# Kernel optimization log

Hardware: AMD Instinct MI355X
Metric: run time of the kernel (lower is better)

The kernel has to match this reference:

```python
import jax, jax.numpy as jnp
import numpy as np

N_HEAD = 12
NEG_INF = -10000.0


def setup_inputs() -> dict:
    key = jax.random.key(0)
    k1, k2, k3 = jax.random.split(key, 3)
    B, S, D = 8, 1024, 768
    std = 0.01
    return {
        "hidden_states": jax.random.normal(k1, (B, S, D), dtype=jnp.float32),
        "Wqkv": jax.random.normal(k2, (D, 3 * D), dtype=jnp.float32) * std,
        "bqkv": jnp.zeros((3 * D,), dtype=jnp.float32),
        "Wout": jax.random.normal(k3, (D, D), dtype=jnp.float32) * std,
        "bout": jnp.zeros((D,), dtype=jnp.float32),
    }


def reference(hidden_states, Wqkv, bqkv, Wout, bout):
    B, S, D = hidden_states.shape
    H = N_HEAD
    hd = D // H
    # fused QKV projection
    qkv = hidden_states @ Wqkv + bqkv  # [B,S,3D]
    qkv = qkv.reshape(B, S, 3, H, hd)
    q, k, v = qkv[:, :, 0], qkv[:, :, 1], qkv[:, :, 2]  # [B,S,H,hd]
    q = q.transpose(0, 2, 1, 3)  # [B,H,S,hd]
    k = k.transpose(0, 2, 1, 3)
    v = v.transpose(0, 2, 1, 3)
    scale = 1.0 / jnp.sqrt(jnp.asarray(hd, dtype=hidden_states.dtype))
    scores = jnp.einsum("bhqd,bhkd->bhqk", q, k) * scale  # [B,H,S,S]
    causal = jnp.tril(jnp.ones((S, S), dtype=bool))[None, None]
    scores = jnp.where(causal, scores, jnp.asarray(NEG_INF, scores.dtype))
    probs = jax.nn.softmax(scores, axis=-1)
    # dropout is identity in eval/deterministic mode
    attn = jnp.einsum("bhqk,bhkd->bhqd", probs, v)  # [B,H,S,hd]
    attn = attn.transpose(0, 2, 1, 3).reshape(B, S, D)
    return attn @ Wout + bout
```

## Files before the change

### kernel.cpp

```cpp
#include <hip/hip_runtime.h>
#include <hip/hip_bf16.h>

#define B_   8
#define S_   1024
#define D_   768
#define H_   12
#define HD_  64
#define BS_  (B_*S_)
#define N3_  (3*D_)

typedef __attribute__((ext_vector_type(8))) short short8;
typedef __attribute__((ext_vector_type(4))) float f32x4;

__device__ __forceinline__ short8 ld8(const __hip_bfloat16* p) {
    return *reinterpret_cast<const short8*>(p);
}
__device__ __forceinline__ void st8(__hip_bfloat16* p, short8 v) {
    *reinterpret_cast<short8*>(p) = v;
}
__device__ __forceinline__ f32x4 mfma16(short8 a, short8 b, f32x4 c) {
    return __builtin_amdgcn_mfma_f32_16x16x32_bf16(a, b, c, 0, 0, 0);
}
__device__ __forceinline__ void async16(const __hip_bfloat16* g, __hip_bfloat16* l) {
    __builtin_amdgcn_global_load_lds((const __attribute__((address_space(1))) void*)g,
                                     (__attribute__((address_space(3))) void*)l,
                                     16, 0, 0);
}
__device__ __forceinline__ float fast_exp2(float x) {
#if __has_builtin(__builtin_amdgcn_exp2f)
    return __builtin_amdgcn_exp2f(x);
#else
    return __expf(x * 0.69314718056f);
#endif
}

__global__ void cast_f32_bf16(const float* __restrict__ in,
                              __hip_bfloat16* __restrict__ out, int n) {
    int i = (blockIdx.x * blockDim.x + threadIdx.x) * 4;
    if (i + 3 < n) {
        float4 v = *reinterpret_cast<const float4*>(in + i);
        out[i + 0] = __float2bfloat16(v.x);
        out[i + 1] = __float2bfloat16(v.y);
        out[i + 2] = __float2bfloat16(v.z);
        out[i + 3] = __float2bfloat16(v.w);
    }
}

__global__ void transpose_cast(const float* __restrict__ in,
                               __hip_bfloat16* __restrict__ out, int R, int C) {
    __shared__ float tile[32][33];
    int c0 = blockIdx.x * 32, r0 = blockIdx.y * 32;
    for (int i = threadIdx.y; i < 32; i += 8) {
        tile[i][threadIdx.x] = in[(size_t)(r0 + i) * C + c0 + threadIdx.x];
    }
    __syncthreads();
    for (int i = threadIdx.y; i < 32; i += 8) {
        out[(size_t)(c0 + i) * R + r0 + threadIdx.x] =
            __float2bfloat16(tile[threadIdx.x][i]);
    }
}

__global__ __launch_bounds__(256)
void gemm_qkv(const __hip_bfloat16* __restrict__ A,
              const __hip_bfloat16* __restrict__ Bt,
              const float* __restrict__ bqkv,
              __hip_bfloat16* __restrict__ Qb,
              __hip_bfloat16* __restrict__ Kb,
              __hip_bfloat16* __restrict__ Vtb) {
    __shared__ __align__(16) char smem[49152];
    __hip_bfloat16* Ct = (__hip_bfloat16*)smem;

    int tid = threadIdx.x, wave = tid >> 6, lane = tid & 63;
    int ln = lane & 15, quad = lane >> 4;
    int mb = blockIdx.y * 128, nb = blockIdx.x * 128;
    int wm = (wave >> 1) * 64, wn = (wave & 1) * 64;

    f32x4 acc[4][4];
#pragma unroll
    for (int i = 0; i < 4; ++i)
#pragma unroll
        for (int j = 0; j < 4; ++j) acc[i][j] = (f32x4){0.f, 0.f, 0.f, 0.f};

    auto stage = [&](int k, int bufoff) {
        __hip_bfloat16* Asb = (__hip_bfloat16*)(smem + bufoff);
        __hip_bfloat16* Bsb = Asb + 128 * 32;
#pragma unroll
        for (int it = 0; it < 2; ++it) {
            int c = it * 256 + tid;
            int row = c >> 2, cc = c & 3;
            int csw = cc ^ ((row >> 1) & 3);
            async16(A + (size_t)(mb + row) * D_ + k + csw * 8,
                    Asb + it * 2048 + wave * 512);
            async16(Bt + (size_t)(nb + row) * D_ + k + csw * 8,
                    Bsb + it * 2048 + wave * 512);
        }
    };

    auto compute = [&](int bufoff) {
        __hip_bfloat16* As = (__hip_bfloat16*)(smem + bufoff);
        __hip_bfloat16* Bs = As + 128 * 32;
        short8 a[4], b[4];
#pragma unroll
        for (int i = 0; i < 4; ++i) {
            int row = wm + i * 16 + ln;
            a[i] = ld8(As + row * 32 + ((quad ^ ((row >> 1) & 3)) << 3));
        }
#pragma unroll
        for (int j = 0; j < 4; ++j) {
            int row = wn + j * 16 + ln;
            b[j] = ld8(Bs + row * 32 + ((quad ^ ((row >> 1) & 3)) << 3));
        }
#pragma unroll
        for (int i = 0; i < 4; ++i)
#pragma unroll
            for (int j = 0; j < 4; ++j)
                acc[i][j] = mfma16(a[i], b[j], acc[i][j]);
    };

    stage(0, 0);
    stage(32, 16384);
    int cb = 0;
    for (int k = 0; k < D_ - 32; k += 32) {
        asm volatile("s_waitcnt vmcnt(4)" ::: "memory");
        asm volatile("s_barrier" ::: "memory");
        if (k + 64 < D_) {
            int sb = cb + 32768; if (sb >= 49152) sb -= 49152;
            stage(k + 64, sb);
        }
        compute(cb);
        cb += 16384; if (cb >= 49152) cb = 0;
    }
    asm volatile("s_waitcnt vmcnt(0)" ::: "memory");
    asm volatile("s_barrier" ::: "memory");
    compute(cb);
    __syncthreads();

    int which = blockIdx.x / 6;
    int nbr = nb - which * D_;
    float qscale = (which == 0) ? (0.125f * 1.44269504089f) : 1.f;

#pragma unroll
    for (int j = 0; j < 4; ++j) {
        int col = wn + j * 16 + ln;
        float bias = bqkv[nb + col];
#pragma unroll
        for (int i = 0; i < 4; ++i)
#pragma unroll
            for (int r = 0; r < 4; ++r) {
                int row = wm + i * 16 + quad * 4 + r;
                __hip_bfloat16 v = __float2bfloat16((acc[i][j][r] + bias) * qscale);
                if (which != 2) Ct[row * 132 + col] = v;
                else            Ct[col * 132 + row] = v;
            }
    }
    __syncthreads();

    int bb = mb >> 10, sb = mb & 1023;
    if (which != 2) {
        __hip_bfloat16* dst = (which == 0) ? Qb : Kb;
#pragma unroll
        for (int it = 0; it < 8; ++it) {
            int cc = it * 256 + tid;
            int row = cc >> 4, c8 = cc & 15;
            short8 v = ld8(Ct + row * 132 + c8 * 8);
            int gcol = nbr + c8 * 8;
            int h = gcol >> 6, d = gcol & 63;
            int s = sb + row;
            st8(dst + (((size_t)(bb * H_ + h)) * S_ + s) * HD_ + d, v);
        }
    } else {
#pragma unroll
        for (int it = 0; it < 8; ++it) {
            int cc = it * 256 + tid;
            int drow = cc >> 4, s8 = cc & 15;
            short8 v = ld8(Ct + drow * 132 + s8 * 8);
            int gd = nbr + drow;
            int h = gd >> 6, d = gd & 63;
            st8(Vtb + ((size_t)(bb * H_ + h) * HD_ + d) * S_ + sb + s8 * 8, v);
        }
    }
}

__global__ __launch_bounds__(256, 3)
void attn_flash3(const __hip_bfloat16* __restrict__ Q,
                 const __hip_bfloat16* __restrict__ K,
                 const __hip_bfloat16* __restrict__ Vt,
                 __hip_bfloat16* __restrict__ attnbf) {
    __shared__ __hip_bfloat16 Kbuf[2][64 * 64];
    __shared__ __hip_bfloat16 Vbuf[2][64 * 64];
    __shared__ __hip_bfloat16 Pbuf[4][32 * 72];

    int bh = blockIdx.y;
    int ip = blockIdx.x;
    int tid = threadIdx.x;
    int wave = tid >> 6, lane = tid & 63;
    int ln = lane & 15, quad = lane >> 4;
    int strip = (wave < 2) ? ip : (15 - ip);
    int qrow0 = strip * 64 + (wave & 1) * 32;

    const __hip_bfloat16* Qbh = Q + (size_t)bh * S_ * HD_;
    const __hip_bfloat16* Kbh = K + (size_t)bh * S_ * HD_;
    const __hip_bfloat16* Vbh = Vt + (size_t)bh * HD_ * S_;

    short8 aq[2][2];
#pragma unroll
    for (int rt = 0; rt < 2; ++rt)
#pragma unroll
        for (int ks = 0; ks < 2; ++ks)
            aq[rt][ks] = ld8(Qbh + (size_t)(qrow0 + rt * 16 + ln) * HD_ +
                             ks * 32 + quad * 8);

    f32x4 o[2][4];
    float l_run[2][4];
#pragma unroll
    for (int rt = 0; rt < 2; ++rt)
#pragma unroll
        for (int n = 0; n < 4; ++n) {
            o[rt][n] = (f32x4){0.f, 0.f, 0.f, 0.f};
            l_run[rt][n] = 0.f;
        }

    int last_kt = 15 - ip;

    auto stage = [&](int kt, int buf) {
        const __hip_bfloat16* gK = Kbh + (size_t)kt * 64 * HD_;
#pragma unroll
        for (int it = 0; it < 2; ++it) {
            int p = it * 256 + tid;
            int row = p >> 3;
            int csw = (p & 7) ^ (row & 7);
            async16(gK + row * HD_ + csw * 8,
                    &Kbuf[buf][it * 2048 + wave * 512]);
            async16(Vbh + (size_t)row * S_ + kt * 64 + csw * 8,
                    &Vbuf[buf][it * 2048 + wave * 512]);
        }
    };

    stage(0, 0);
    __syncthreads();
    int cur = 0;

    for (int kt = 0; kt <= last_kt; ++kt) {
        int kbase = kt * 64;
        if (kt < last_kt) stage(kt + 1, cur ^ 1);

        if (kbase <= qrow0 + 31) {
            const __hip_bfloat16* Kc = Kbuf[cur];
            const __hip_bfloat16* Vc = Vbuf[cur];

            f32x4 s[2][4];
#pragma unroll
            for (int rt = 0; rt < 2; ++rt)
#pragma unroll
                for (int j = 0; j < 4; ++j) s[rt][j] = (f32x4){0.f, 0.f, 0.f, 0.f};
#pragma unroll
            for (int j = 0; j < 4; ++j) {
                int row = j * 16 + ln;
#pragma unroll
                for (int ks = 0; ks < 2; ++ks) {
                    short8 bk = ld8(&Kc[row * 64 +
                                        (((ks * 4 + quad) ^ (row & 7)) << 3)]);
#pragma unroll
                    for (int rt = 0; rt < 2; ++rt)
                        s[rt][j] = mfma16(aq[rt][ks], bk, s[rt][j]);
                }
            }

            if (kbase + 63 > qrow0) {
#pragma unroll
                for (int rt = 0; rt < 2; ++rt)
#pragma unroll
                    for (int j = 0; j < 4; ++j) {
                        int key = kbase + j * 16 + ln;
#pragma unroll
                        for (int r = 0; r < 4; ++r) {
                            int q = qrow0 + rt * 16 + quad * 4 + r;
                            if (key > q) s[rt][j][r] = -INFINITY;
                        }
                    }
            }

#pragma unroll
            for (int rt = 0; rt < 2; ++rt)
#pragma unroll
                for (int j = 0; j < 4; ++j)
#pragma unroll
                    for (int r = 0; r < 4; ++r)
                        s[rt][j][r] = fast_exp2(s[rt][j][r]);
#pragma unroll
            for (int rt = 0; rt < 2; ++rt)
#pragma unroll
                for (int r = 0; r < 4; ++r)
                    l_run[rt][r] += (s[rt][0][r] + s[rt][1][r]) +
                                    (s[rt][2][r] + s[rt][3][r]);

#pragma unroll
            for (int rt = 0; rt < 2; ++rt)
#pragma unroll
                for (int j = 0; j < 4; ++j)
#pragma unroll
                    for (int r = 0; r < 4; ++r)
                        Pbuf[wave][(rt * 16 + quad * 4 + r) * 72 + j * 16 + ln] =
                            __float2bfloat16(s[rt][j][r]);
            asm volatile("s_waitcnt lgkmcnt(0)" ::: "memory");

            short8 ap[2][2];
#pragma unroll
            for (int rt = 0; rt < 2; ++rt)
#pragma unroll
                for (int ks = 0; ks < 2; ++ks)
                    ap[rt][ks] = ld8(&Pbuf[wave][(rt * 16 + ln) * 72 +
                                                 ks * 32 + quad * 8]);

#pragma unroll
            for (int n = 0; n < 4; ++n) {
                int row = n * 16 + ln;
#pragma unroll
                for (int ks = 0; ks < 2; ++ks) {
                    short8 bv = ld8(&Vc[row * 64 +
                                        (((ks * 4 + quad) ^ (row & 7)) << 3)]);
#pragma unroll
                    for (int rt = 0; rt < 2; ++rt)
                        o[rt][n] = mfma16(ap[rt][ks], bv, o[rt][n]);
                }
            }
        }

        __syncthreads();
        cur ^= 1;
    }

    int bb = bh / H_, h = bh - bb * H_;
#pragma unroll
    for (int rt = 0; rt < 2; ++rt)
#pragma unroll
        for (int r = 0; r < 4; ++r) {
            float l = l_run[rt][r];
            l += __shfl_xor(l, 1);
            l += __shfl_xor(l, 2);
            l += __shfl_xor(l, 4);
            l += __shfl_xor(l, 8);
            float inv = 1.f / l;
            int row = qrow0 + rt * 16 + quad * 4 + r;
#pragma unroll
            for (int n = 0; n < 4; ++n) {
                int col = h * 64 + n * 16 + ln;
                attnbf[((size_t)bb * S_ + row) * D_ + col] =
                    __float2bfloat16(o[rt][n][r] * inv);
            }
        }
}

__global__ __launch_bounds__(256)
void gemm_out(const __hip_bfloat16* __restrict__ A,
              const __hip_bfloat16* __restrict__ Bt,
              const float* __restrict__ bias,
              float* __restrict__ Cout) {
    __shared__ __align__(16) char smem[49152];

    int tid = threadIdx.x, wave = tid >> 6, lane = tid & 63;
    int ln = lane & 15, quad = lane >> 4;
    int mb = blockIdx.y * 128, nb = blockIdx.x * 128;
    int wm = (wave >> 1) * 64, wn = (wave & 1) * 64;

    f32x4 acc[4][4];
#pragma unroll
    for (int i = 0; i < 4; ++i)
#pragma unroll
        for (int j = 0; j < 4; ++j) acc[i][j] = (f32x4){0.f, 0.f, 0.f, 0.f};

    auto stage = [&](int k, int bufoff) {
        __hip_bfloat16* Asb = (__hip_bfloat16*)(smem + bufoff);
        __hip_bfloat16* Bsb = Asb + 128 * 32;
#pragma unroll
        for (int it = 0; it < 2; ++it) {
            int c = it * 256 + tid;
            int row = c >> 2, cc = c & 3;
            int csw = cc ^ ((row >> 1) & 3);
            async16(A + (size_t)(mb + row) * D_ + k + csw * 8,
                    Asb + it * 2048 + wave * 512);
            async16(Bt + (size_t)(nb + row) * D_ + k + csw * 8,
                    Bsb + it * 2048 + wave * 512);
        }
    };

    auto compute = [&](int bufoff) {
        __hip_bfloat16* As = (__hip_bfloat16*)(smem + bufoff);
        __hip_bfloat16* Bs = As + 128 * 32;
        short8 a[4], b[4];
#pragma unroll
        for (int i = 0; i < 4; ++i) {
            int row = wm + i * 16 + ln;
            a[i] = ld8(As + row * 32 + ((quad ^ ((row >> 1) & 3)) << 3));
        }
#pragma unroll
        for (int j = 0; j < 4; ++j) {
            int row = wn + j * 16 + ln;
            b[j] = ld8(Bs + row * 32 + ((quad ^ ((row >> 1) & 3)) << 3));
        }
#pragma unroll
        for (int i = 0; i < 4; ++i)
#pragma unroll
            for (int j = 0; j < 4; ++j)
                acc[i][j] = mfma16(a[i], b[j], acc[i][j]);
    };

    stage(0, 0);
    stage(32, 16384);
    int cb = 0;
    for (int k = 0; k < D_ - 32; k += 32) {
        asm volatile("s_waitcnt vmcnt(4)" ::: "memory");
        asm volatile("s_barrier" ::: "memory");
        if (k + 64 < D_) {
            int sb = cb + 32768; if (sb >= 49152) sb -= 49152;
            stage(k + 64, sb);
        }
        compute(cb);
        cb += 16384; if (cb >= 49152) cb = 0;
    }
    asm volatile("s_waitcnt vmcnt(0)" ::: "memory");
    asm volatile("s_barrier" ::: "memory");
    compute(cb);

#pragma unroll
    for (int j = 0; j < 4; ++j) {
        int col = nb + wn + j * 16 + ln;
        float bv = bias[col];
#pragma unroll
        for (int i = 0; i < 4; ++i)
#pragma unroll
            for (int r = 0; r < 4; ++r) {
                int row = mb + wm + i * 16 + quad * 4 + r;
                Cout[(size_t)row * D_ + col] = acc[i][j][r] + bv;
            }
    }
}

extern "C" void kernel_launch(void* const* d_in, const int* in_sizes, int n_in,
                              void* d_out, int out_size, void* d_ws, size_t ws_size,
                              hipStream_t stream) {
    const float* X    = (const float*)d_in[0];
    const float* Wqkv = (const float*)d_in[1];
    const float* bqkv = (const float*)d_in[2];
    const float* Wout = (const float*)d_in[3];
    const float* bout = (const float*)d_in[4];
    float* out = (float*)d_out;

    constexpr size_t SZ_XBF   = (size_t)BS_ * D_ * 2;
    constexpr size_t SZ_WQKVT = (size_t)N3_ * D_ * 2;
    constexpr size_t SZ_WOUTT = (size_t)D_ * D_ * 2;
    constexpr size_t SZ_QKV   = (size_t)B_ * H_ * S_ * HD_ * 2;

    char* w = (char*)d_ws;
    __hip_bfloat16* Xbf    = (__hip_bfloat16*)(w);
    __hip_bfloat16* WqkvT  = (__hip_bfloat16*)(w + SZ_XBF);
    __hip_bfloat16* WoutT  = (__hip_bfloat16*)(w + SZ_XBF + SZ_WQKVT);
    __hip_bfloat16* Qb     = (__hip_bfloat16*)(w + SZ_XBF + SZ_WQKVT + SZ_WOUTT);
    __hip_bfloat16* Kb     = (__hip_bfloat16*)(w + SZ_XBF + SZ_WQKVT + SZ_WOUTT + SZ_QKV);
    __hip_bfloat16* Vtb    = (__hip_bfloat16*)(w + SZ_XBF + SZ_WQKVT + SZ_WOUTT + 2*SZ_QKV);
    __hip_bfloat16* attnbf = (__hip_bfloat16*)(w + SZ_XBF + SZ_WQKVT + SZ_WOUTT + 3*SZ_QKV);
    (void)ws_size; (void)in_sizes; (void)n_in; (void)out_size;

    int nX = BS_ * D_;
    cast_f32_bf16<<<nX / (256 * 4), 256, 0, stream>>>(X, Xbf, nX);
    transpose_cast<<<dim3(N3_ / 32, D_ / 32), dim3(32, 8), 0, stream>>>(Wqkv, WqkvT, D_, N3_);
    transpose_cast<<<dim3(D_ / 32, D_ / 32), dim3(32, 8), 0, stream>>>(Wout, WoutT, D_, D_);

    gemm_qkv<<<dim3(N3_ / 128, BS_ / 128), 256, 0, stream>>>(Xbf, WqkvT, bqkv, Qb, Kb, Vtb);

    attn_flash3<<<dim3(8, B_ * H_), 256, 0, stream>>>(Qb, Kb, Vtb, attnbf);

    gemm_out<<<dim3(D_ / 128, BS_ / 128), 256, 0, stream>>>(attnbf, WoutT, bout, out);
}
```

Before: 191.1 us.

## Share 256x128 GEMM core with 8 waves, BK=64, triple-buffered ping-pong schedule

Both projection GEMMs now call a shared core that uses 512-thread blocks computing 256x128 tiles with a K-step of 64, triple-buffered LDS (144KB) and an XOR swizzle over 8 chunks. Each K-step is split into two halves separated by barriers, with s_setprio around the MFMA bursts so loads from one wave group overlap with compute from another. This is meant to raise data reuse per block and hide global-load latency better than the earlier 128x128 double/triple-buffered loop. The cost is large LDS use, which limits blocks per CU to one, plus more barriers per step. The epilogue for the transposed V store is widened to match the taller tile.

Result: no change. 193.3 us (+1.1%).

```diff
diff --git a/kernel.cpp b/kernel.cpp
--- a/kernel.cpp
+++ b/kernel.cpp
@@ -60,79 +60,136 @@
     }
 }
 
-__global__ __launch_bounds__(256)
+__device__ __forceinline__ void gemm_core(const __hip_bfloat16* __restrict__ A,
+                                          const __hip_bfloat16* __restrict__ Bt,
+                                          char* smem, int mb, int nb,
+                                          int tid, f32x4 acc[4][4]) {
+    const int wave = tid >> 6, lane = tid & 63;
+    const int ln = lane & 15, quad = lane >> 4;
+    const int wm = (wave >> 1) * 64, wn = (wave & 1) * 64;
+
+#pragma unroll
+    for (int i = 0; i < 4; ++i)
+#pragma unroll
+        for (int j = 0; j < 4; ++j) acc[i][j] = (f32x4){0.f, 0.f, 0.f, 0.f};
+
+    auto stageA3 = [&](int kt, char* base) {
+#pragma unroll
+        for (int ld = 0; ld < 3; ++ld) {
+            int q = ld * 512 + tid;
+            int row = q >> 3;
+            int ck = (q & 7) ^ (row & 7);
+            async16(A + (size_t)(mb + row) * D_ + kt * 64 + ck * 8,
+                    (__hip_bfloat16*)(base + ld * 8192 + wave * 1024));
+        }
+    };
+    auto stageA1B2 = [&](int kt, char* base) {
+        {
+            int q = 3 * 512 + tid;
+            int row = q >> 3;
+            int ck = (q & 7) ^ (row & 7);
+            async16(A + (size_t)(mb + row) * D_ + kt * 64 + ck * 8,
+                    (__hip_bfloat16*)(base + 3 * 8192 + wave * 1024));
+        }
+#pragma unroll
+        for (int ld = 0; ld < 2; ++ld) {
+            int q = ld * 512 + tid;
+            int row = q >> 3;
+            int ck = (q & 7) ^ (row & 7);
+            async16(Bt + (size_t)(nb + row) * D_ + kt * 64 + ck * 8,
+                    (__hip_bfloat16*)(base + 32768 + ld * 8192 + wave * 1024));
+        }
+    };
+
+    stageA3(0, smem);          stageA1B2(0, smem);
+    stageA3(1, smem + 49152);  stageA1B2(1, smem + 49152);
+    asm volatile("s_waitcnt vmcnt(6)" ::: "memory");
+    asm volatile("s_barrier" ::: "memory");
+
+#pragma unroll
+    for (int t = 0; t < 12; ++t) {
+        char* cur = smem + (t % 3) * 49152;
+        char* nxt = smem + ((t + 2) % 3) * 49152;
+        const __hip_bfloat16* As = (const __hip_bfloat16*)cur;
+        const __hip_bfloat16* Bs = (const __hip_bfloat16*)(cur + 32768);
+
+        short8 a[4][2], b0[2][2], b1[2][2];
+
+#pragma unroll
+        for (int i = 0; i < 4; ++i) {
+            int row = wm + i * 16 + ln;
+#pragma unroll
+            for (int ks = 0; ks < 2; ++ks)
+                a[i][ks] = ld8(As + row * 64 + (((ks * 4 + quad) ^ (row & 7)) << 3));
+        }
+#pragma unroll
+        for (int j = 0; j < 2; ++j) {
+            int row = wn + j * 16 + ln;
+#pragma unroll
+            for (int ks = 0; ks < 2; ++ks)
+                b0[j][ks] = ld8(Bs + row * 64 + (((ks * 4 + quad) ^ (row & 7)) << 3));
+        }
+        if (t + 2 < 12) stageA3(t + 2, nxt);
+        asm volatile("s_barrier" ::: "memory");
+        asm volatile("s_waitcnt lgkmcnt(0)" ::: "memory");
+        __builtin_amdgcn_sched_barrier(0);
+        __builtin_amdgcn_s_setprio(1);
+#pragma unroll
+        for (int ks = 0; ks < 2; ++ks)
+#pragma unroll
+            for (int i = 0; i < 4; ++i) {
+                acc[i][0] = mfma16(a[i][ks], b0[0][ks], acc[i][0]);
+                acc[i][1] = mfma16(a[i][ks], b0[1][ks], acc[i][1]);
+            }
+        __builtin_amdgcn_s_setprio(0);
+        asm volatile("s_barrier" ::: "memory");
+
+#pragma unroll
+        for (int j = 0; j < 2; ++j) {
+            int row = wn + (2 + j) * 16 + ln;
+#pragma unroll
+            for (int ks = 0; ks < 2; ++ks)
+                b1[j][ks] = ld8(Bs + row * 64 + (((ks * 4 + quad) ^ (row & 7)) << 3));
+        }
+        if (t + 2 < 12) stageA1B2(t + 2, nxt);
+        if (t < 10) {
+            asm volatile("s_waitcnt vmcnt(6)" ::: "memory");
+        } else if (t == 10) {
+            asm volatile("s_waitcnt vmcnt(0)" ::: "memory");
+        }
+        asm volatile("s_barrier" ::: "memory");
+        asm volatile("s_waitcnt lgkmcnt(0)" ::: "memory");
+        __builtin_amdgcn_sched_barrier(0);
+        __builtin_amdgcn_s_setprio(1);
+#pragma unroll
+        for (int ks = 0; ks < 2; ++ks)
+#pragma unroll
+            for (int i = 0; i < 4; ++i) {
+                acc[i][2] = mfma16(a[i][ks], b1[0][ks], acc[i][2]);
+                acc[i][3] = mfma16(a[i][ks], b1[1][ks], acc[i][3]);
+            }
+        __builtin_amdgcn_s_setprio(0);
+        asm volatile("s_barrier" ::: "memory");
+    }
+}
+
+__global__ __launch_bounds__(512)
 void gemm_qkv(const __hip_bfloat16* __restrict__ A,
               const __hip_bfloat16* __restrict__ Bt,
               const float* __restrict__ bqkv,
               __hip_bfloat16* __restrict__ Qb,
               __hip_bfloat16* __restrict__ Kb,
               __hip_bfloat16* __restrict__ Vtb) {
-    __shared__ __align__(16) char smem[49152];
+    __shared__ __align__(16) char smem[3 * 49152];
     __hip_bfloat16* Ct = (__hip_bfloat16*)smem;
 
     int tid = threadIdx.x, wave = tid >> 6, lane = tid & 63;
     int ln = lane & 15, quad = lane >> 4;
-    int mb = blockIdx.y * 128, nb = blockIdx.x * 128;
+    int mb = blockIdx.y * 256, nb = blockIdx.x * 128;
     int wm = (wave >> 1) * 64, wn = (wave & 1) * 64;
 
     f32x4 acc[4][4];
-#pragma unroll
-    for (int i = 0; i < 4; ++i)
-#pragma unroll
-        for (int j = 0; j < 4; ++j) acc[i][j] = (f32x4){0.f, 0.f, 0.f, 0.f};
-
-    auto stage = [&](int k, int bufoff) {
-        __hip_bfloat16* Asb = (__hip_bfloat16*)(smem + bufoff);
-        __hip_bfloat16* Bsb = Asb + 128 * 32;
-#pragma unroll
-        for (int it = 0; it < 2; ++it) {
-            int c = it * 256 + tid;
-            int row = c >> 2, cc = c & 3;
-            int csw = cc ^ ((row >> 1) & 3);
-            async16(A + (size_t)(mb + row) * D_ + k + csw * 8,
-                    Asb + it * 2048 + wave * 512);
-            async16(Bt + (size_t)(nb + row) * D_ + k + csw * 8,
-                    Bsb + it * 2048 + wave * 512);
-        }
-    };
-
-    auto compute = [&](int bufoff) {
-        __hip_bfloat16* As = (__hip_bfloat16*)(smem + bufoff);
-        __hip_bfloat16* Bs = As + 128 * 32;
-        short8 a[4], b[4];
-#pragma unroll
-        for (int i = 0; i < 4; ++i) {
-            int row = wm + i * 16 + ln;
-            a[i] = ld8(As + row * 32 + ((quad ^ ((row >> 1) & 3)) << 3));
-        }
-#pragma unroll
-        for (int j = 0; j < 4; ++j) {
-            int row = wn + j * 16 + ln;
-            b[j] = ld8(Bs + row * 32 + ((quad ^ ((row >> 1) & 3)) << 3));
-        }
-#pragma unroll
-        for (int i = 0; i < 4; ++i)
-#pragma unroll
-            for (int j = 0; j < 4; ++j)
-                acc[i][j] = mfma16(a[i], b[j], acc[i][j]);
-    };
-
-    stage(0, 0);
-    stage(32, 16384);
-    int cb = 0;
-    for (int k = 0; k < D_ - 32; k += 32) {
-        asm volatile("s_waitcnt vmcnt(4)" ::: "memory");
-        asm volatile("s_barrier" ::: "memory");
-        if (k + 64 < D_) {
-            int sb = cb + 32768; if (sb >= 49152) sb -= 49152;
-            stage(k + 64, sb);
-        }
-        compute(cb);
-        cb += 16384; if (cb >= 49152) cb = 0;
-    }
-    asm volatile("s_waitcnt vmcnt(0)" ::: "memory");
-    asm volatile("s_barrier" ::: "memory");
-    compute(cb);
+    gemm_core(A, Bt, smem, mb, nb, tid, acc);
     __syncthreads();
 
     int which = blockIdx.x / 6;
@@ -150,7 +207,7 @@
                 int row = wm + i * 16 + quad * 4 + r;
                 __hip_bfloat16 v = __float2bfloat16((acc[i][j][r] + bias) * qscale);
                 if (which != 2) Ct[row * 132 + col] = v;
-                else            Ct[col * 132 + row] = v;
+                else            Ct[col * 264 + row] = v;
             }
     }
     __syncthreads();
@@ -160,7 +217,7 @@
         __hip_bfloat16* dst = (which == 0) ? Qb : Kb;
 #pragma unroll
         for (int it = 0; it < 8; ++it) {
-            int cc = it * 256 + tid;
+            int cc = it * 512 + tid;
             int row = cc >> 4, c8 = cc & 15;
             short8 v = ld8(Ct + row * 132 + c8 * 8);
             int gcol = nbr + c8 * 8;
@@ -171,9 +228,9 @@
     } else {
 #pragma unroll
         for (int it = 0; it < 8; ++it) {
-            int cc = it * 256 + tid;
-            int drow = cc >> 4, s8 = cc & 15;
-            short8 v = ld8(Ct + drow * 132 + s8 * 8);
+            int cc = it * 512 + tid;
+            int drow = cc >> 5, s8 = cc & 31;
+            short8 v = ld8(Ct + drow * 264 + s8 * 8);
             int gd = nbr + drow;
             int h = gd >> 6, d = gd & 63;
             st8(Vtb + ((size_t)(bb * H_ + h) * HD_ + d) * S_ + sb + s8 * 8, v);
@@ -351,76 +408,20 @@
         }
 }
 
-__global__ __launch_bounds__(256)
+__global__ __launch_bounds__(512)
 void gemm_out(const __hip_bfloat16* __restrict__ A,
               const __hip_bfloat16* __restrict__ Bt,
               const float* __restrict__ bias,
               float* __restrict__ Cout) {
-    __shared__ __align__(16) char smem[49152];
+    __shared__ __align__(16) char smem[3 * 49152];
 
     int tid = threadIdx.x, wave = tid >> 6, lane = tid & 63;
     int ln = lane & 15, quad = lane >> 4;
-    int mb = blockIdx.y * 128, nb = blockIdx.x * 128;
+    int mb = blockIdx.y * 256, nb = blockIdx.x * 128;
     int wm = (wave >> 1) * 64, wn = (wave & 1) * 64;
 
     f32x4 acc[4][4];
-#pragma unroll
-    for (int i = 0; i < 4; ++i)
-#pragma unroll
-        for (int j = 0; j < 4; ++j) acc[i][j] = (f32x4){0.f, 0.f, 0.f, 0.f};
-
-    auto stage = [&](int k, int bufoff) {
-        __hip_bfloat16* Asb = (__hip_bfloat16*)(smem + bufoff);
-        __hip_bfloat16* Bsb = Asb + 128 * 32;
-#pragma unroll
-        for (int it = 0; it < 2; ++it) {
-            int c = it * 256 + tid;
-            int row = c >> 2, cc = c & 3;
-            int csw = cc ^ ((row >> 1) & 3);
-            async16(A + (size_t)(mb + row) * D_ + k + csw * 8,
-                    Asb + it * 2048 + wave * 512);
-            async16(Bt + (size_t)(nb + row) * D_ + k + csw * 8,
-                    Bsb + it * 2048 + wave * 512);
-        }
-    };
-
-    auto compute = [&](int bufoff) {
-        __hip_bfloat16* As = (__hip_bfloat16*)(smem + bufoff);
-        __hip_bfloat16* Bs = As + 128 * 32;
-        short8 a[4], b[4];
-#pragma unroll
-        for (int i = 0; i < 4; ++i) {
-            int row = wm + i * 16 + ln;
-            a[i] = ld8(As + row * 32 + ((quad ^ ((row >> 1) & 3)) << 3));
-        }
-#pragma unroll
-        for (int j = 0; j < 4; ++j) {
-            int row = wn + j * 16 + ln;
-            b[j] = ld8(Bs + row * 32 + ((quad ^ ((row >> 1) & 3)) << 3));
-        }
-#pragma unroll
-        for (int i = 0; i < 4; ++i)
-#pragma unroll
-            for (int j = 0; j < 4; ++j)
-                acc[i][j] = mfma16(a[i], b[j], acc[i][j]);
-    };
-
-    stage(0, 0);
-    stage(32, 16384);
-    int cb = 0;
-    for (int k = 0; k < D_ - 32; k += 32) {
-        asm volatile("s_waitcnt vmcnt(4)" ::: "memory");
-        asm volatile("s_barrier" ::: "memory");
-        if (k + 64 < D_) {
-            int sb = cb + 32768; if (sb >= 49152) sb -= 49152;
-            stage(k + 64, sb);
-        }
-        compute(cb);
-        cb += 16384; if (cb >= 49152) cb = 0;
-    }
-    asm volatile("s_waitcnt vmcnt(0)" ::: "memory");
-    asm volatile("s_barrier" ::: "memory");
-    compute(cb);
+    gemm_core(A, Bt, smem, mb, nb, tid, acc);
 
 #pragma unroll
     for (int j = 0; j < 4; ++j) {
@@ -466,9 +467,9 @@
     transpose_cast<<<dim3(N3_ / 32, D_ / 32), dim3(32, 8), 0, stream>>>(Wqkv, WqkvT, D_, N3_);
     transpose_cast<<<dim3(D_ / 32, D_ / 32), dim3(32, 8), 0, stream>>>(Wout, WoutT, D_, D_);
 
-    gemm_qkv<<<dim3(N3_ / 128, BS_ / 128), 256, 0, stream>>>(Xbf, WqkvT, bqkv, Qb, Kb, Vtb);
+    gemm_qkv<<<dim3(N3_ / 128, BS_ / 256), 512, 0, stream>>>(Xbf, WqkvT, bqkv, Qb, Kb, Vtb);
 
     attn_flash3<<<dim3(8, B_ * H_), 256, 0, stream>>>(Qb, Kb, Vtb, attnbf);
 
-    gemm_out<<<dim3(D_ / 128, BS_ / 128), 256, 0, stream>>>(attnbf, WoutT, bout, out);
-}
+    gemm_out<<<dim3(D_ / 128, BS_ / 256), 512, 0, stream>>>(attnbf, WoutT, bout, out);
+}
```
